# Kernel tuning notes

Measured on AMD Instinct MI355X. Metric: run time of the kernel, lower is better.

The kernel has to match this reference:

```python
import jax, jax.numpy as jnp
import numpy as np

D_MODEL, N_HEAD, HEAD_SIZE = 1024, 16, 64
NEG_INF = -1e30


def setup_inputs() -> dict:
    key = jax.random.key(0)
    ks = jax.random.split(key, 12)
    B, S = 4, 4096
    w = 0.02
    return {
        "query": jax.random.normal(ks[0], (B, S, D_MODEL), jnp.float32),
        "key":   jax.random.normal(ks[1], (B, S, D_MODEL), jnp.float32),
        "value": jax.random.normal(ks[2], (B, S, D_MODEL), jnp.float32),
        "mask":  jnp.ones((HEAD_SIZE, HEAD_SIZE), jnp.int32),
        "Wq": jax.random.normal(ks[3], (D_MODEL, HEAD_SIZE), jnp.float32) * w,
        "bq": jnp.zeros((HEAD_SIZE,), jnp.float32),
        "Wk": jax.random.normal(ks[4], (D_MODEL, HEAD_SIZE), jnp.float32) * w,
        "bk": jnp.zeros((HEAD_SIZE,), jnp.float32),
        "Wv": jax.random.normal(ks[5], (D_MODEL, HEAD_SIZE), jnp.float32) * w,
        "bv": jnp.zeros((HEAD_SIZE,), jnp.float32),
        "Wp": jax.random.normal(ks[6], (D_MODEL, D_MODEL), jnp.float32) * w,
        "bp": jnp.zeros((D_MODEL,), jnp.float32),
    }


def reference(query, key, value, mask, Wq, bq, Wk, bk, Wv, bv, Wp, bp):
    h, dh = N_HEAD, HEAD_SIZE
    # Linear projections: (B,S,d_model) -> (B,S,head_size)
    q = query @ Wq + bq
    k = key @ Wk + bk
    v = value @ Wv + bv
    # Faithful to torch: view(-1, h, dh).transpose(1,2) on (B,S,head_size)
    # -> (N, dh, h) with N = B*S/h
    q = q.reshape(-1, h, dh).transpose(0, 2, 1)
    k = k.reshape(-1, h, dh).transpose(0, 2, 1)
    v = v.reshape(-1, h, dh).transpose(0, 2, 1)
    scale = q.shape[-1] ** (-0.5)  # dhead = h in the original code
    # scores: (N, dh, dh)
    scores = jnp.einsum('nik,njk->nij', q, k) * scale
    scores = jnp.where(mask == 0, NEG_INF, scores)
    # NOTE: original code computes softmax(scores) but then overwrites it;
    # the actual output uses dropout(raw scores) @ v. Dropout in eval = identity.
    x = jnp.einsum('nij,njh->nih', scores, v)  # (N, dh, h)
    x = x.transpose(0, 2, 1).reshape(-1, h * dh)  # (N, d_model)
    return x @ Wp + bp
```

## Files before the change

kernel.cpp:

```cpp
#include <hip/hip_runtime.h>
#include <hip/hip_bf16.h>
#include <stdint.h>


typedef float f32x4 __attribute__((ext_vector_type(4)));
typedef short s16x8 __attribute__((ext_vector_type(8)));

#define T_TOK 16384
#define KDIM  1024
#define HS    64

__device__ __forceinline__ short f2bf(float f) {
    union { float f; uint32_t u; } x; x.f = f;
    uint32_t u = x.u;
    u += 0x7FFFu + ((u >> 16) & 1u);
    return (short)(u >> 16);
}

__global__ __launch_bounds__(256) void wtrans_kernel(
    const float* __restrict__ Wq, const float* __restrict__ Wk,
    const float* __restrict__ Wv, const float* __restrict__ Wp,
    short* __restrict__ Wtq, short* __restrict__ Wtk,
    short* __restrict__ Wtv, short* __restrict__ Wpt)
{
    const int bid = blockIdx.x;
    const float* src; short* dst; int N, k0, n0;
    if (bid < 256) { src = Wp; dst = Wpt; N = 1024; k0 = (bid >> 4) * 64; n0 = (bid & 15) * 64; }
    else {
        int r = bid - 256; int p = r >> 4;
        src = (p == 0) ? Wq : (p == 1) ? Wk : Wv;
        dst = (p == 0) ? Wtq : (p == 1) ? Wtk : Wtv;
        N = 64; k0 = (r & 15) * 64; n0 = 0;
    }
    __shared__ float Ts[64][68];
    const int tid = threadIdx.x;
    #pragma unroll
    for (int i = 0; i < 4; ++i) {
        int idx = i * 256 + tid;
        int r = idx >> 4, c4 = idx & 15;
        f32x4 v = *(const f32x4*)&src[(size_t)(k0 + r) * N + n0 + c4 * 4];
        *(f32x4*)&Ts[r][c4 * 4] = v;
    }
    __syncthreads();
    #pragma unroll
    for (int i = 0; i < 2; ++i) {
        int idx = i * 256 + tid;
        int n = idx >> 3, c8 = idx & 7;
        s16x8 h;
        #pragma unroll
        for (int j = 0; j < 8; ++j) h[j] = f2bf(Ts[c8 * 8 + j][n]);
        *(s16x8*)&dst[(size_t)(n0 + n) * KDIM + k0 + c8 * 8] = h;
    }
}

__global__ __launch_bounds__(256, 2) void qkv_proj_kernel(
    const float* __restrict__ Q, const float* __restrict__ K,
    const float* __restrict__ V,
    const short* __restrict__ Wtq, const short* __restrict__ Wtk,
    const short* __restrict__ Wtv,
    const float* __restrict__ bq, const float* __restrict__ bk,
    const float* __restrict__ bv,
    float* __restrict__ OutQKV)
{
    const int p = blockIdx.y;
    const float* In = (p == 0) ? Q : (p == 1) ? K : V;
    const short* Wt = (p == 0) ? Wtq : (p == 1) ? Wtk : Wtv;
    const float* bb = (p == 0) ? bq : (p == 1) ? bk : bv;
    float* Out = OutQKV + (size_t)p * T_TOK * HS;

    const int tid  = threadIdx.x;
    const int wave = tid >> 6;
    const int lane = tid & 63;
    const int lhi  = lane >> 4;
    const int llo  = lane & 15;
    const int n0   = wave * 16;
    const int t0   = blockIdx.x * 64;

    s16x8 breg[32];
    const short* bptr = Wt + (size_t)(n0 + llo) * KDIM + lhi * 8;
    #pragma unroll
    for (int i = 0; i < 32; ++i) breg[i] = *(const s16x8*)(bptr + i * 32);

    const float bias = bb[n0 + llo];

    for (int t = 0; t < 4; ++t) {
        const float* ap = In + (size_t)(t0 + t * 16 + llo) * KDIM + lhi * 8;
        f32x4 acc = {};
        #pragma unroll
        for (int i = 0; i < 32; ++i) {
            f32x4 a0 = *(const f32x4*)(ap + i * 32);
            f32x4 a1 = *(const f32x4*)(ap + i * 32 + 4);
            s16x8 af;
            af[0] = f2bf(a0.x); af[1] = f2bf(a0.y); af[2] = f2bf(a0.z); af[3] = f2bf(a0.w);
            af[4] = f2bf(a1.x); af[5] = f2bf(a1.y); af[6] = f2bf(a1.z); af[7] = f2bf(a1.w);
            acc = __builtin_amdgcn_mfma_f32_16x16x32_bf16(af, breg[i], acc, 0, 0, 0);
        }
        #pragma unroll
        for (int r = 0; r < 4; ++r)
            Out[(size_t)(t0 + t * 16 + lhi * 4 + r) * HS + n0 + llo] = acc[r] + bias;
    }
}

__global__ __launch_bounds__(256) void group_attn_kernel(
    const float* __restrict__ QKV, short* __restrict__ Xbf)
{
    const int n = blockIdx.x;
    __shared__ float Sq[16][68];
    __shared__ float Sk[16][68];
    __shared__ float Sv[16][68];
    __shared__ float KV[16][17];

    const int tid = threadIdx.x;
    const float* qp = QKV + (size_t)n * 16 * HS;
    const float* kp = qp + (size_t)T_TOK * HS;
    const float* vp = kp + (size_t)T_TOK * HS;

    #pragma unroll
    for (int i = 0; i < 4; ++i) {
        int idx = i * 256 + tid;
        int row = idx >> 6, c = idx & 63;
        Sq[row][c] = qp[idx];
        Sk[row][c] = kp[idx];
        Sv[row][c] = vp[idx];
    }
    __syncthreads();

    {
        int b = tid >> 4, a = tid & 15;
        const f32x4* kb = (const f32x4*)&Sk[b][0];
        const f32x4* va = (const f32x4*)&Sv[a][0];
        float s = 0.f;
        #pragma unroll
        for (int j = 0; j < 16; ++j) {
            f32x4 x = kb[j], y = va[j];
            s += x.x * y.x + x.y * y.y + x.z * y.z + x.w * y.w;
        }
        KV[b][a] = s * 0.25f;
    }
    __syncthreads();

    const int i = tid & 63;
    const int w = tid >> 6;
    float qv[16];
    #pragma unroll
    for (int b = 0; b < 16; ++b) qv[b] = Sq[b][i];
    #pragma unroll
    for (int u = 0; u < 4; ++u) {
        int a = u * 4 + w;
        float s = 0.f;
        #pragma unroll
        for (int b = 0; b < 16; ++b) s += qv[b] * KV[b][a];
        Xbf[(size_t)n * 1024 + a * 64 + i] = f2bf(s);
    }
}

__global__ __launch_bounds__(256, 2) void out_proj_kernel(
    const short* __restrict__ Xbf, const short* __restrict__ Wpt,
    const float* __restrict__ bp, float* __restrict__ Out)
{
    const int tid  = threadIdx.x;
    const int wave = tid >> 6;
    const int lane = tid & 63;
    const int lhi  = lane >> 4, llo = lane & 15;
    const int n0   = blockIdx.x * 64 + wave * 16;
    const int m0   = blockIdx.y * 32;

    s16x8 breg[32];
    const short* bptr = Wpt + (size_t)(n0 + llo) * KDIM + lhi * 8;
    #pragma unroll
    for (int i = 0; i < 32; ++i) breg[i] = *(const s16x8*)(bptr + i * 32);

    const float bias = bp[n0 + llo];

    #pragma unroll
    for (int t = 0; t < 2; ++t) {
        const short* ap = Xbf + (size_t)(m0 + t * 16 + llo) * KDIM + lhi * 8;
        f32x4 acc = {};
        #pragma unroll
        for (int i = 0; i < 32; ++i) {
            s16x8 a = *(const s16x8*)(ap + i * 32);
            acc = __builtin_amdgcn_mfma_f32_16x16x32_bf16(a, breg[i], acc, 0, 0, 0);
        }
        #pragma unroll
        for (int r = 0; r < 4; ++r)
            Out[(size_t)(m0 + t * 16 + lhi * 4 + r) * KDIM + n0 + llo] = acc[r] + bias;
    }
}

extern "C" void kernel_launch(void* const* d_in, const int* in_sizes, int n_in,
                              void* d_out, int out_size, void* d_ws, size_t ws_size,
                              hipStream_t stream) {
    const float* Q  = (const float*)d_in[0];
    const float* K  = (const float*)d_in[1];
    const float* V  = (const float*)d_in[2];
    const float* Wq = (const float*)d_in[4];
    const float* bq = (const float*)d_in[5];
    const float* Wk = (const float*)d_in[6];
    const float* bk = (const float*)d_in[7];
    const float* Wv = (const float*)d_in[8];
    const float* bv = (const float*)d_in[9];
    const float* Wp = (const float*)d_in[10];
    const float* bp = (const float*)d_in[11];
    float* out = (float*)d_out;

    char* ws = (char*)d_ws;
    float* qkv = (float*)ws;
    size_t off = (size_t)3 * T_TOK * HS * sizeof(float);
    short* Xbf = (short*)(ws + off); off += (size_t)1024 * 1024 * 2;
    short* Wtq = (short*)(ws + off); off += (size_t)HS * KDIM * 2;
    short* Wtk = (short*)(ws + off); off += (size_t)HS * KDIM * 2;
    short* Wtv = (short*)(ws + off); off += (size_t)HS * KDIM * 2;
    short* Wpt = (short*)(ws + off); off += (size_t)KDIM * KDIM * 2;

    wtrans_kernel<<<dim3(304), 256, 0, stream>>>(Wq, Wk, Wv, Wp, Wtq, Wtk, Wtv, Wpt);
    qkv_proj_kernel<<<dim3(T_TOK / 64, 3), 256, 0, stream>>>(
        Q, K, V, Wtq, Wtk, Wtv, bq, bk, bv, qkv);
    group_attn_kernel<<<dim3(1024), 256, 0, stream>>>(qkv, Xbf);
    out_proj_kernel<<<dim3(16, 32), 256, 0, stream>>>(Xbf, Wpt, bp, out);
}
```

Before: 298.9 us.

## Stage GEMM operands through double-buffered LDS with async global-to-LDS loads

Result: faster. 242.8 us (-18.8%).

```diff
diff --git a/kernel.cpp b/kernel.cpp
--- a/kernel.cpp
+++ b/kernel.cpp
@@ -15,6 +15,12 @@
     uint32_t u = x.u;
     u += 0x7FFFu + ((u >> 16) & 1u);
     return (short)(u >> 16);
+}
+
+__device__ __forceinline__ void gl2lds16(const void* g, void* l) {
+    __builtin_amdgcn_global_load_lds(
+        (const __attribute__((address_space(1))) void*)g,
+        (__attribute__((address_space(3))) void*)l, 16, 0, 0);
 }
 
 __global__ __launch_bounds__(256) void wtrans_kernel(
@@ -53,7 +59,7 @@
     }
 }
 
-__global__ __launch_bounds__(256, 2) void qkv_proj_kernel(
+__global__ __launch_bounds__(256) void qkv_proj_kernel(
     const float* __restrict__ Q, const float* __restrict__ K,
     const float* __restrict__ V,
     const short* __restrict__ Wtq, const short* __restrict__ Wtk,
@@ -68,37 +74,68 @@
     const float* bb = (p == 0) ? bq : (p == 1) ? bk : bv;
     float* Out = OutQKV + (size_t)p * T_TOK * HS;
 
+    __shared__ __align__(16) char lds[2][16384];
+
     const int tid  = threadIdx.x;
     const int wave = tid >> 6;
     const int lane = tid & 63;
     const int lhi  = lane >> 4;
     const int llo  = lane & 15;
-    const int n0   = wave * 16;
-    const int t0   = blockIdx.x * 64;
-
-    s16x8 breg[32];
-    const short* bptr = Wt + (size_t)(n0 + llo) * KDIM + lhi * 8;
-    #pragma unroll
-    for (int i = 0; i < 32; ++i) breg[i] = *(const s16x8*)(bptr + i * 32);
-
-    const float bias = bb[n0 + llo];
-
-    for (int t = 0; t < 4; ++t) {
-        const float* ap = In + (size_t)(t0 + t * 16 + llo) * KDIM + lhi * 8;
-        f32x4 acc = {};
-        #pragma unroll
-        for (int i = 0; i < 32; ++i) {
-            f32x4 a0 = *(const f32x4*)(ap + i * 32);
-            f32x4 a1 = *(const f32x4*)(ap + i * 32 + 4);
-            s16x8 af;
-            af[0] = f2bf(a0.x); af[1] = f2bf(a0.y); af[2] = f2bf(a0.z); af[3] = f2bf(a0.w);
-            af[4] = f2bf(a1.x); af[5] = f2bf(a1.y); af[6] = f2bf(a1.z); af[7] = f2bf(a1.w);
-            acc = __builtin_amdgcn_mfma_f32_16x16x32_bf16(af, breg[i], acc, 0, 0, 0);
+    const int t0   = blockIdx.x * 32;
+
+    int oA0 = (wave * 2 + 0) * 1024 + lane * 16;
+    int oA1 = (wave * 2 + 1) * 1024 + lane * 16;
+    int rA0 = oA0 >> 8, pA0 = (oA0 >> 4) & 15;
+    int rA1 = oA1 >> 8, pA1 = (oA1 >> 4) & 15;
+    size_t gA0 = (size_t)(t0 + rA0) * KDIM + (((pA0 >> 1) ^ (rA0 & 7)) * 8 + (pA0 & 1) * 4);
+    size_t gA1 = (size_t)(t0 + rA1) * KDIM + (((pA1 >> 1) ^ (rA1 & 7)) * 8 + (pA1 & 1) * 4);
+    int oB0 = (wave * 2 + 0) * 1024 + lane * 16;
+    int oB1 = (wave * 2 + 1) * 1024 + lane * 16;
+    int rB0 = oB0 >> 7, qB0 = (oB0 >> 4) & 7;
+    int rB1 = oB1 >> 7, qB1 = (oB1 >> 4) & 7;
+    size_t gB0 = (size_t)rB0 * KDIM + ((qB0 ^ (rB0 & 7)) * 8);
+    size_t gB1 = (size_t)rB1 * KDIM + ((qB1 ^ (rB1 & 7)) * 8);
+
+    f32x4 acc[2] = {};
+
+    #define STAGE(b, kk)  do {                                   \
+        gl2lds16(In + gA0 + (kk), &lds[b][oA0]);                 \
+        gl2lds16(In + gA1 + (kk), &lds[b][oA1]);                 \
+        gl2lds16(Wt + gB0 + (kk), &lds[b][8192 + oB0]);          \
+        gl2lds16(Wt + gB1 + (kk), &lds[b][8192 + oB1]);          \
+    } while (0)
+
+    STAGE(0, 0);
+    for (int c = 0; c < 16; ++c) {
+        __syncthreads();
+        if (c < 15) STAGE((c + 1) & 1, (c + 1) * 64);
+        const char* Ab = lds[c & 1];
+        const char* Bb = lds[c & 1] + 8192;
+        #pragma unroll
+        for (int hh = 0; hh < 2; ++hh) {
+            int pB = (hh * 4 + lhi) ^ (llo & 7);
+            s16x8 bf = *(const s16x8*)(Bb + (wave * 16 + llo) * 128 + pB * 16);
+            #pragma unroll
+            for (int tt = 0; tt < 2; ++tt) {
+                int r = tt * 16 + llo;
+                int pA = (hh * 4 + lhi) ^ (llo & 7);
+                const f32x4* ap = (const f32x4*)(Ab + r * 256 + pA * 32);
+                f32x4 a0 = ap[0], a1 = ap[1];
+                s16x8 af;
+                af[0] = f2bf(a0.x); af[1] = f2bf(a0.y); af[2] = f2bf(a0.z); af[3] = f2bf(a0.w);
+                af[4] = f2bf(a1.x); af[5] = f2bf(a1.y); af[6] = f2bf(a1.z); af[7] = f2bf(a1.w);
+                acc[tt] = __builtin_amdgcn_mfma_f32_16x16x32_bf16(af, bf, acc[tt], 0, 0, 0);
+            }
         }
+    }
+    #undef STAGE
+
+    const float bias = bb[wave * 16 + llo];
+    #pragma unroll
+    for (int tt = 0; tt < 2; ++tt)
         #pragma unroll
         for (int r = 0; r < 4; ++r)
-            Out[(size_t)(t0 + t * 16 + lhi * 4 + r) * HS + n0 + llo] = acc[r] + bias;
-    }
+            Out[(size_t)(t0 + tt * 16 + lhi * 4 + r) * HS + wave * 16 + llo] = acc[tt][r] + bias;
 }
 
 __global__ __launch_bounds__(256) void group_attn_kernel(
@@ -115,13 +152,11 @@
     const float* kp = qp + (size_t)T_TOK * HS;
     const float* vp = kp + (size_t)T_TOK * HS;
 
-    #pragma unroll
-    for (int i = 0; i < 4; ++i) {
-        int idx = i * 256 + tid;
-        int row = idx >> 6, c = idx & 63;
-        Sq[row][c] = qp[idx];
-        Sk[row][c] = kp[idx];
-        Sv[row][c] = vp[idx];
+    {
+        int row = tid >> 4, c4 = (tid & 15) * 4;
+        *(f32x4*)&Sq[row][c4] = *(const f32x4*)&qp[tid * 4];
+        *(f32x4*)&Sk[row][c4] = *(const f32x4*)&kp[tid * 4];
+        *(f32x4*)&Sv[row][c4] = *(const f32x4*)&vp[tid * 4];
     }
     __syncthreads();
 
@@ -154,37 +189,65 @@
     }
 }
 
-__global__ __launch_bounds__(256, 2) void out_proj_kernel(
+__global__ __launch_bounds__(256) void out_proj_kernel(
     const short* __restrict__ Xbf, const short* __restrict__ Wpt,
     const float* __restrict__ bp, float* __restrict__ Out)
 {
+    __shared__ __align__(16) char lds[2][12288];
+
     const int tid  = threadIdx.x;
     const int wave = tid >> 6;
     const int lane = tid & 63;
     const int lhi  = lane >> 4, llo = lane & 15;
-    const int n0   = blockIdx.x * 64 + wave * 16;
+    const int n0   = blockIdx.x * 64;
     const int m0   = blockIdx.y * 32;
 
-    s16x8 breg[32];
-    const short* bptr = Wpt + (size_t)(n0 + llo) * KDIM + lhi * 8;
-    #pragma unroll
-    for (int i = 0; i < 32; ++i) breg[i] = *(const s16x8*)(bptr + i * 32);
-
-    const float bias = bp[n0 + llo];
-
-    #pragma unroll
-    for (int t = 0; t < 2; ++t) {
-        const short* ap = Xbf + (size_t)(m0 + t * 16 + llo) * KDIM + lhi * 8;
-        f32x4 acc = {};
-        #pragma unroll
-        for (int i = 0; i < 32; ++i) {
-            s16x8 a = *(const s16x8*)(ap + i * 32);
-            acc = __builtin_amdgcn_mfma_f32_16x16x32_bf16(a, breg[i], acc, 0, 0, 0);
+    int oA = wave * 1024 + lane * 16;
+    int rA = oA >> 7, qA = (oA >> 4) & 7;
+    size_t gA = (size_t)(m0 + rA) * KDIM + ((qA ^ (rA & 7)) * 8);
+    int oB0 = (wave * 2 + 0) * 1024 + lane * 16;
+    int oB1 = (wave * 2 + 1) * 1024 + lane * 16;
+    int rB0 = oB0 >> 7, qB0 = (oB0 >> 4) & 7;
+    int rB1 = oB1 >> 7, qB1 = (oB1 >> 4) & 7;
+    size_t gB0 = (size_t)(n0 + rB0) * KDIM + ((qB0 ^ (rB0 & 7)) * 8);
+    size_t gB1 = (size_t)(n0 + rB1) * KDIM + ((qB1 ^ (rB1 & 7)) * 8);
+
+    f32x4 acc[2] = {};
+
+    #define STAGE3(b, kk) do {                                    \
+        gl2lds16(Xbf + gA  + (kk), &lds[b][oA]);                  \
+        gl2lds16(Wpt + gB0 + (kk), &lds[b][4096 + oB0]);          \
+        gl2lds16(Wpt + gB1 + (kk), &lds[b][4096 + oB1]);          \
+    } while (0)
+
+    STAGE3(0, 0);
+    for (int c = 0; c < 16; ++c) {
+        __syncthreads();
+        if (c < 15) STAGE3((c + 1) & 1, (c + 1) * 64);
+        const char* Ab = lds[c & 1];
+        const char* Bb = lds[c & 1] + 4096;
+        #pragma unroll
+        for (int hh = 0; hh < 2; ++hh) {
+            int pB = (hh * 4 + lhi) ^ (llo & 7);
+            s16x8 bf = *(const s16x8*)(Bb + (wave * 16 + llo) * 128 + pB * 16);
+            #pragma unroll
+            for (int tt = 0; tt < 2; ++tt) {
+                int r = tt * 16 + llo;
+                int pA = (hh * 4 + lhi) ^ (llo & 7);
+                s16x8 af = *(const s16x8*)(Ab + r * 128 + pA * 16);
+                acc[tt] = __builtin_amdgcn_mfma_f32_16x16x32_bf16(af, bf, acc[tt], 0, 0, 0);
+            }
         }
+    }
+    #undef STAGE3
+
+    const float bias = bp[n0 + wave * 16 + llo];
+    #pragma unroll
+    for (int tt = 0; tt < 2; ++tt)
         #pragma unroll
         for (int r = 0; r < 4; ++r)
-            Out[(size_t)(m0 + t * 16 + lhi * 4 + r) * KDIM + n0 + llo] = acc[r] + bias;
-    }
+            Out[(size_t)(m0 + tt * 16 + lhi * 4 + r) * KDIM + n0 + wave * 16 + llo]
+                = acc[tt][r] + bias;
 }
 
 extern "C" void kernel_launch(void* const* d_in, const int* in_sizes, int n_in,
@@ -213,7 +276,7 @@
     short* Wpt = (short*)(ws + off); off += (size_t)KDIM * KDIM * 2;
 
     wtrans_kernel<<<dim3(304), 256, 0, stream>>>(Wq, Wk, Wv, Wp, Wtq, Wtk, Wtv, Wpt);
-    qkv_proj_kernel<<<dim3(T_TOK / 64, 3), 256, 0, stream>>>(
+    qkv_proj_kernel<<<dim3(T_TOK / 32, 3), 256, 0, stream>>>(
         Q, K, V, Wtq, Wtk, Wtv, bq, bk, bv, qkv);
     group_attn_kernel<<<dim3(1024), 256, 0, stream>>>(qkv, Xbf);
     out_proj_kernel<<<dim3(16, 32), 256, 0, stream>>>(Xbf, Wpt, bp, out);
```

## Stage weights in swizzled LDS and give each wave full-width output tiles

Applied to the files above, without the earlier changes.

Result: faster. 253.9 us (-15.1%).

```diff
diff --git a/kernel.cpp b/kernel.cpp
--- a/kernel.cpp
+++ b/kernel.cpp
@@ -68,36 +68,71 @@
     const float* bb = (p == 0) ? bq : (p == 1) ? bk : bv;
     float* Out = OutQKV + (size_t)p * T_TOK * HS;
 
+    __shared__ short Bs[64 * 512];
+
     const int tid  = threadIdx.x;
     const int wave = tid >> 6;
     const int lane = tid & 63;
     const int lhi  = lane >> 4;
     const int llo  = lane & 15;
-    const int n0   = wave * 16;
     const int t0   = blockIdx.x * 64;
 
-    s16x8 breg[32];
-    const short* bptr = Wt + (size_t)(n0 + llo) * KDIM + lhi * 8;
-    #pragma unroll
-    for (int i = 0; i < 32; ++i) breg[i] = *(const s16x8*)(bptr + i * 32);
-
-    const float bias = bb[n0 + llo];
-
-    for (int t = 0; t < 4; ++t) {
-        const float* ap = In + (size_t)(t0 + t * 16 + llo) * KDIM + lhi * 8;
-        f32x4 acc = {};
-        #pragma unroll
-        for (int i = 0; i < 32; ++i) {
-            f32x4 a0 = *(const f32x4*)(ap + i * 32);
-            f32x4 a1 = *(const f32x4*)(ap + i * 32 + 4);
-            s16x8 af;
-            af[0] = f2bf(a0.x); af[1] = f2bf(a0.y); af[2] = f2bf(a0.z); af[3] = f2bf(a0.w);
-            af[4] = f2bf(a1.x); af[5] = f2bf(a1.y); af[6] = f2bf(a1.z); af[7] = f2bf(a1.w);
-            acc = __builtin_amdgcn_mfma_f32_16x16x32_bf16(af, breg[i], acc, 0, 0, 0);
-        }
+    const float* ap_base = In + (size_t)(t0 + wave * 16 + llo) * KDIM + lhi * 8;
+
+    f32x4 acc[4] = {};
+
+    for (int kh = 0; kh < 2; ++kh) {
+        __syncthreads();
+        #pragma unroll
+        for (int i = 0; i < 16; ++i) {
+            int G = i * 256 + tid;
+            int r = G >> 6, g = G & 63;
+            s16x8 w = *(const s16x8*)&Wt[(size_t)r * KDIM + kh * 512 + g * 8];
+            *(s16x8*)&Bs[r * 512 + (g ^ (r & 7)) * 8] = w;
+        }
+        __syncthreads();
+
+        const float* ap = ap_base + kh * 512;
+        f32x4 abuf[2][4][2];
+        #pragma unroll
+        for (int c = 0; c < 4; ++c) {
+            abuf[0][c][0] = *(const f32x4*)(ap + c * 32);
+            abuf[0][c][1] = *(const f32x4*)(ap + c * 32 + 4);
+        }
+        for (int o = 0; o < 4; ++o) {
+            const int pp = o & 1;
+            if (o < 3) {
+                const float* apn = ap + (o + 1) * 128;
+                #pragma unroll
+                for (int c = 0; c < 4; ++c) {
+                    abuf[pp ^ 1][c][0] = *(const f32x4*)(apn + c * 32);
+                    abuf[pp ^ 1][c][1] = *(const f32x4*)(apn + c * 32 + 4);
+                }
+            }
+            #pragma unroll
+            for (int c = 0; c < 4; ++c) {
+                f32x4 a0 = abuf[pp][c][0], a1 = abuf[pp][c][1];
+                s16x8 af;
+                af[0] = f2bf(a0.x); af[1] = f2bf(a0.y); af[2] = f2bf(a0.z); af[3] = f2bf(a0.w);
+                af[4] = f2bf(a1.x); af[5] = f2bf(a1.y); af[6] = f2bf(a1.z); af[7] = f2bf(a1.w);
+                const int gk = o * 16 + c * 4 + lhi;
+                #pragma unroll
+                for (int nt = 0; nt < 4; ++nt) {
+                    int n = nt * 16 + llo;
+                    s16x8 bf = *(const s16x8*)&Bs[n * 512 + (gk ^ (n & 7)) * 8];
+                    acc[nt] = __builtin_amdgcn_mfma_f32_16x16x32_bf16(af, bf, acc[nt], 0, 0, 0);
+                }
+            }
+        }
+    }
+
+    #pragma unroll
+    for (int nt = 0; nt < 4; ++nt) {
+        const int col = nt * 16 + llo;
+        const float bias = bb[col];
         #pragma unroll
         for (int r = 0; r < 4; ++r)
-            Out[(size_t)(t0 + t * 16 + lhi * 4 + r) * HS + n0 + llo] = acc[r] + bias;
+            Out[(size_t)(t0 + wave * 16 + lhi * 4 + r) * HS + col] = acc[nt][r] + bias;
     }
 }
 
@@ -115,13 +150,11 @@
     const float* kp = qp + (size_t)T_TOK * HS;
     const float* vp = kp + (size_t)T_TOK * HS;
 
-    #pragma unroll
-    for (int i = 0; i < 4; ++i) {
-        int idx = i * 256 + tid;
-        int row = idx >> 6, c = idx & 63;
-        Sq[row][c] = qp[idx];
-        Sk[row][c] = kp[idx];
-        Sv[row][c] = vp[idx];
+    {
+        int row = tid >> 4, c4 = (tid & 15) * 4;
+        *(f32x4*)&Sq[row][c4] = *(const f32x4*)&qp[tid * 4];
+        *(f32x4*)&Sk[row][c4] = *(const f32x4*)&kp[tid * 4];
+        *(f32x4*)&Sv[row][c4] = *(const f32x4*)&vp[tid * 4];
     }
     __syncthreads();
 
@@ -158,32 +191,61 @@
     const short* __restrict__ Xbf, const short* __restrict__ Wpt,
     const float* __restrict__ bp, float* __restrict__ Out)
 {
+    __shared__ short Bs[64 * 512];
+
     const int tid  = threadIdx.x;
     const int wave = tid >> 6;
     const int lane = tid & 63;
     const int lhi  = lane >> 4, llo = lane & 15;
-    const int n0   = blockIdx.x * 64 + wave * 16;
-    const int m0   = blockIdx.y * 32;
-
-    s16x8 breg[32];
-    const short* bptr = Wpt + (size_t)(n0 + llo) * KDIM + lhi * 8;
-    #pragma unroll
-    for (int i = 0; i < 32; ++i) breg[i] = *(const s16x8*)(bptr + i * 32);
-
-    const float bias = bp[n0 + llo];
-
-    #pragma unroll
-    for (int t = 0; t < 2; ++t) {
-        const short* ap = Xbf + (size_t)(m0 + t * 16 + llo) * KDIM + lhi * 8;
-        f32x4 acc = {};
-        #pragma unroll
-        for (int i = 0; i < 32; ++i) {
-            s16x8 a = *(const s16x8*)(ap + i * 32);
-            acc = __builtin_amdgcn_mfma_f32_16x16x32_bf16(a, breg[i], acc, 0, 0, 0);
-        }
+    const int m0   = blockIdx.x * 64;
+    const int n0   = blockIdx.y * 64;
+
+    const short* ap_base = Xbf + (size_t)(m0 + wave * 16 + llo) * KDIM + lhi * 8;
+
+    f32x4 acc[4] = {};
+
+    for (int kh = 0; kh < 2; ++kh) {
+        __syncthreads();
+        #pragma unroll
+        for (int i = 0; i < 16; ++i) {
+            int G = i * 256 + tid;
+            int r = G >> 6, g = G & 63;
+            s16x8 w = *(const s16x8*)&Wpt[(size_t)(n0 + r) * KDIM + kh * 512 + g * 8];
+            *(s16x8*)&Bs[r * 512 + (g ^ (r & 7)) * 8] = w;
+        }
+        __syncthreads();
+
+        const short* ap = ap_base + kh * 512;
+        s16x8 abuf[2][4];
+        #pragma unroll
+        for (int c = 0; c < 4; ++c) abuf[0][c] = *(const s16x8*)(ap + c * 32);
+        for (int o = 0; o < 4; ++o) {
+            const int pp = o & 1;
+            if (o < 3) {
+                const short* apn = ap + (o + 1) * 128;
+                #pragma unroll
+                for (int c = 0; c < 4; ++c) abuf[pp ^ 1][c] = *(const s16x8*)(apn + c * 32);
+            }
+            #pragma unroll
+            for (int c = 0; c < 4; ++c) {
+                const int gk = o * 16 + c * 4 + lhi;
+                #pragma unroll
+                for (int nt = 0; nt < 4; ++nt) {
+                    int n = nt * 16 + llo;
+                    s16x8 bf = *(const s16x8*)&Bs[n * 512 + (gk ^ (n & 7)) * 8];
+                    acc[nt] = __builtin_amdgcn_mfma_f32_16x16x32_bf16(abuf[pp][c], bf, acc[nt], 0, 0, 0);
+                }
+            }
+        }
+    }
+
+    #pragma unroll
+    for (int nt = 0; nt < 4; ++nt) {
+        const int col = n0 + nt * 16 + llo;
+        const float bias = bp[col];
         #pragma unroll
         for (int r = 0; r < 4; ++r)
-            Out[(size_t)(m0 + t * 16 + lhi * 4 + r) * KDIM + n0 + llo] = acc[r] + bias;
+            Out[(size_t)(m0 + wave * 16 + lhi * 4 + r) * KDIM + col] = acc[nt][r] + bias;
     }
 }
 
@@ -216,5 +278,5 @@
     qkv_proj_kernel<<<dim3(T_TOK / 64, 3), 256, 0, stream>>>(
         Q, K, V, Wtq, Wtk, Wtv, bq, bk, bv, qkv);
     group_attn_kernel<<<dim3(1024), 256, 0, stream>>>(qkv, Xbf);
-    out_proj_kernel<<<dim3(16, 32), 256, 0, stream>>>(Xbf, Wpt, bp, out);
-}
+    out_proj_kernel<<<dim3(16, 16), 256, 0, stream>>>(Xbf, Wpt, bp, out);
+}
```

## Stream GEMM A-tiles through LDS with async global_load_lds multi-buffering

Applied to the files above, without the earlier changes.

New measurement: 250.3 us. -16.3%, faster.

```diff
diff --git a/kernel.cpp b/kernel.cpp
--- a/kernel.cpp
+++ b/kernel.cpp
@@ -15,6 +15,21 @@
     uint32_t u = x.u;
     u += 0x7FFFu + ((u >> 16) & 1u);
     return (short)(u >> 16);
+}
+
+__device__ __forceinline__ void gl2lds16(const void* g, void* l) {
+    __builtin_amdgcn_global_load_lds(
+        (const __attribute__((address_space(1))) void*)g,
+        (__attribute__((address_space(3))) void*)l, 16, 0, 0);
+}
+
+__device__ __forceinline__ void wait_vm(int n) {
+    if (n >= 12)      asm volatile("s_waitcnt vmcnt(12)" ::: "memory");
+    else if (n == 8)  asm volatile("s_waitcnt vmcnt(8)"  ::: "memory");
+    else if (n == 6)  asm volatile("s_waitcnt vmcnt(6)"  ::: "memory");
+    else if (n == 4)  asm volatile("s_waitcnt vmcnt(4)"  ::: "memory");
+    else if (n == 2)  asm volatile("s_waitcnt vmcnt(2)"  ::: "memory");
+    else              asm volatile("s_waitcnt vmcnt(0)"  ::: "memory");
 }
 
 __global__ __launch_bounds__(256) void wtrans_kernel(
@@ -68,37 +83,68 @@
     const float* bb = (p == 0) ? bq : (p == 1) ? bk : bv;
     float* Out = OutQKV + (size_t)p * T_TOK * HS;
 
+    __shared__ __align__(16) char lds[4][16384];
+
     const int tid  = threadIdx.x;
     const int wave = tid >> 6;
     const int lane = tid & 63;
     const int lhi  = lane >> 4;
     const int llo  = lane & 15;
+    const int t0   = blockIdx.x * 64;
     const int n0   = wave * 16;
-    const int t0   = blockIdx.x * 64;
+    char* ldsw = &lds[wave][0];
 
     s16x8 breg[32];
-    const short* bptr = Wt + (size_t)(n0 + llo) * KDIM + lhi * 8;
-    #pragma unroll
-    for (int i = 0; i < 32; ++i) breg[i] = *(const s16x8*)(bptr + i * 32);
-
+    const short* wp = Wt + (size_t)(n0 + llo) * KDIM + lhi * 8;
+    #pragma unroll
+    for (int i = 0; i < 32; ++i) breg[i] = *(const s16x8*)(wp + i * 32);
     const float bias = bb[n0 + llo];
 
-    for (int t = 0; t < 4; ++t) {
-        const float* ap = In + (size_t)(t0 + t * 16 + llo) * KDIM + lhi * 8;
-        f32x4 acc = {};
-        #pragma unroll
-        for (int i = 0; i < 32; ++i) {
-            f32x4 a0 = *(const f32x4*)(ap + i * 32);
-            f32x4 a1 = *(const f32x4*)(ap + i * 32 + 4);
+    int aoff[4];
+    #pragma unroll
+    for (int j = 0; j < 4; ++j) {
+        int rj = j * 4 + (lane >> 4);
+        aoff[j] = rj * KDIM + ((((lane & 15) >> 1) ^ (rj & 7)) * 8 + (lane & 1) * 4);
+    }
+    const int ldst = lane * 16;
+
+    #define ISSUE_Q(u) do {                                                     \
+        const float* _b = In + (size_t)t0 * KDIM                                \
+                          + ((u) >> 4) * 16 * KDIM + ((u) & 15) * 64;           \
+        char* _d = ldsw + ((u) & 3) * 4096;                                     \
+        gl2lds16(_b + aoff[0], _d + 0 * 1024 + ldst);                           \
+        gl2lds16(_b + aoff[1], _d + 1 * 1024 + ldst);                           \
+        gl2lds16(_b + aoff[2], _d + 2 * 1024 + ldst);                           \
+        gl2lds16(_b + aoff[3], _d + 3 * 1024 + ldst);                           \
+    } while (0)
+
+    ISSUE_Q(0); ISSUE_Q(1); ISSUE_Q(2); ISSUE_Q(3);
+
+    f32x4 acc = {};
+    #pragma unroll
+    for (int u = 0; u < 64; ++u) {
+        wait_vm(u <= 60 ? 12 : (63 - u) * 4);
+        const char* slot = ldsw + (u & 3) * 4096;
+        #pragma unroll
+        for (int s = 0; s < 2; ++s) {
+            int pos = (s * 4 + lhi) ^ (llo & 7);
+            const f32x4* ap = (const f32x4*)(slot + llo * 256 + pos * 32);
+            f32x4 a0 = ap[0], a1 = ap[1];
             s16x8 af;
             af[0] = f2bf(a0.x); af[1] = f2bf(a0.y); af[2] = f2bf(a0.z); af[3] = f2bf(a0.w);
             af[4] = f2bf(a1.x); af[5] = f2bf(a1.y); af[6] = f2bf(a1.z); af[7] = f2bf(a1.w);
-            acc = __builtin_amdgcn_mfma_f32_16x16x32_bf16(af, breg[i], acc, 0, 0, 0);
-        }
-        #pragma unroll
-        for (int r = 0; r < 4; ++r)
-            Out[(size_t)(t0 + t * 16 + lhi * 4 + r) * HS + n0 + llo] = acc[r] + bias;
-    }
+            acc = __builtin_amdgcn_mfma_f32_16x16x32_bf16(af, breg[(u & 15) * 2 + s], acc, 0, 0, 0);
+        }
+        if (u + 4 < 64) ISSUE_Q(u + 4);
+        if ((u & 15) == 15) {
+            const int row0 = t0 + (u >> 4) * 16 + lhi * 4;
+            #pragma unroll
+            for (int r = 0; r < 4; ++r)
+                Out[(size_t)(row0 + r) * HS + n0 + llo] = acc[r] + bias;
+            acc = (f32x4){};
+        }
+    }
+    #undef ISSUE_Q
 }
 
 __global__ __launch_bounds__(256) void group_attn_kernel(
@@ -115,13 +161,11 @@
     const float* kp = qp + (size_t)T_TOK * HS;
     const float* vp = kp + (size_t)T_TOK * HS;
 
-    #pragma unroll
-    for (int i = 0; i < 4; ++i) {
-        int idx = i * 256 + tid;
-        int row = idx >> 6, c = idx & 63;
-        Sq[row][c] = qp[idx];
-        Sk[row][c] = kp[idx];
-        Sv[row][c] = vp[idx];
+    {
+        int row = tid >> 4, c4 = (tid & 15) * 4;
+        *(f32x4*)&Sq[row][c4] = *(const f32x4*)&qp[tid * 4];
+        *(f32x4*)&Sk[row][c4] = *(const f32x4*)&kp[tid * 4];
+        *(f32x4*)&Sv[row][c4] = *(const f32x4*)&vp[tid * 4];
     }
     __syncthreads();
 
@@ -158,33 +202,61 @@
     const short* __restrict__ Xbf, const short* __restrict__ Wpt,
     const float* __restrict__ bp, float* __restrict__ Out)
 {
+    __shared__ __align__(16) char lds[4][8192];
+
     const int tid  = threadIdx.x;
     const int wave = tid >> 6;
     const int lane = tid & 63;
     const int lhi  = lane >> 4, llo = lane & 15;
     const int n0   = blockIdx.x * 64 + wave * 16;
     const int m0   = blockIdx.y * 32;
+    char* ldsw = &lds[wave][0];
 
     s16x8 breg[32];
-    const short* bptr = Wpt + (size_t)(n0 + llo) * KDIM + lhi * 8;
-    #pragma unroll
-    for (int i = 0; i < 32; ++i) breg[i] = *(const s16x8*)(bptr + i * 32);
-
+    const short* wp = Wpt + (size_t)(n0 + llo) * KDIM + lhi * 8;
+    #pragma unroll
+    for (int i = 0; i < 32; ++i) breg[i] = *(const s16x8*)(wp + i * 32);
     const float bias = bp[n0 + llo];
 
-    #pragma unroll
-    for (int t = 0; t < 2; ++t) {
-        const short* ap = Xbf + (size_t)(m0 + t * 16 + llo) * KDIM + lhi * 8;
-        f32x4 acc = {};
-        #pragma unroll
-        for (int i = 0; i < 32; ++i) {
-            s16x8 a = *(const s16x8*)(ap + i * 32);
-            acc = __builtin_amdgcn_mfma_f32_16x16x32_bf16(a, breg[i], acc, 0, 0, 0);
-        }
-        #pragma unroll
-        for (int r = 0; r < 4; ++r)
-            Out[(size_t)(m0 + t * 16 + lhi * 4 + r) * KDIM + n0 + llo] = acc[r] + bias;
-    }
+    int aoff[2];
+    #pragma unroll
+    for (int j = 0; j < 2; ++j) {
+        int rj = j * 8 + (lane >> 3);
+        aoff[j] = rj * KDIM + ((lane & 7) ^ (rj & 7)) * 8;
+    }
+    const int ldst = lane * 16;
+
+    #define ISSUE_O(u) do {                                                     \
+        const short* _b = Xbf + (size_t)m0 * KDIM                               \
+                          + ((u) >> 4) * 16 * KDIM + ((u) & 15) * 64;           \
+        char* _d = ldsw + ((u) & 3) * 2048;                                     \
+        gl2lds16(_b + aoff[0], _d + 0 * 1024 + ldst);                           \
+        gl2lds16(_b + aoff[1], _d + 1 * 1024 + ldst);                           \
+    } while (0)
+
+    ISSUE_O(0); ISSUE_O(1); ISSUE_O(2); ISSUE_O(3);
+
+    f32x4 acc = {};
+    #pragma unroll
+    for (int u = 0; u < 32; ++u) {
+        wait_vm(u <= 28 ? 6 : (31 - u) * 2);
+        const char* slot = ldsw + (u & 3) * 2048;
+        #pragma unroll
+        for (int s = 0; s < 2; ++s) {
+            int pos = (s * 4 + lhi) ^ (llo & 7);
+            s16x8 af = *(const s16x8*)(slot + llo * 128 + pos * 16);
+            acc = __builtin_amdgcn_mfma_f32_16x16x32_bf16(af, breg[(u & 15) * 2 + s], acc, 0, 0, 0);
+        }
+        if (u + 4 < 32) ISSUE_O(u + 4);
+        if ((u & 15) == 15) {
+            const int row0 = m0 + (u >> 4) * 16 + lhi * 4;
+            #pragma unroll
+            for (int r = 0; r < 4; ++r)
+                Out[(size_t)(row0 + r) * KDIM + n0 + llo] = acc[r] + bias;
+            acc = (f32x4){};
+        }
+    }
+    #undef ISSUE_O
 }
 
 extern "C" void kernel_launch(void* const* d_in, const int* in_sizes, int n_in,
```
